# Kernel tuning notes

Measured on AMD Instinct MI355X. Metric: run time of the kernel, lower is better.

The kernel has to match this reference:

```python
import jax, jax.numpy as jnp
import numpy as np

MAX_STEPS = 50
B, H, A = 4096, 1024, 128


def setup_inputs() -> dict:
    key = jax.random.key(0)
    ks = jax.random.split(key, 7)
    s = 1.0 / np.sqrt(H)  # torch default LSTM/Linear init scale
    return {
        "encoder_output": jax.random.normal(ks[0], (1, B, H), dtype=jnp.float32),
        "w_ih": jax.random.normal(ks[1], (4 * H, H), dtype=jnp.float32) * s,
        "w_hh": jax.random.normal(ks[2], (4 * H, H), dtype=jnp.float32) * s,
        "b_ih": jax.random.normal(ks[3], (4 * H,), dtype=jnp.float32) * s,
        "b_hh": jax.random.normal(ks[4], (4 * H,), dtype=jnp.float32) * s,
        "w_pred": jax.random.normal(ks[5], (A, H), dtype=jnp.float32) * s,
        "b_pred": jax.random.normal(ks[6], (A,), dtype=jnp.float32) * s,
    }


def reference(encoder_output, w_ih, w_hh, b_ih, b_hh, w_pred, b_pred):
    # LSTM output (hidden state) of step t; seq_len is always 1.
    hidden = w_hh.shape[1]
    x0 = encoder_output[0]                        # (B, H)
    h0 = jnp.zeros_like(x0)
    c0 = jnp.zeros_like(x0)
    bias = b_ih + b_hh                            # (4H,)

    def step(carry, _):
        x, h, c = carry
        gates = x @ w_ih.T + h @ w_hh.T + bias    # (B, 4H)
        i, f, g, o = jnp.split(gates, 4, axis=-1)  # torch gate order i,f,g,o
        c_new = jax.nn.sigmoid(f) * c + jax.nn.sigmoid(i) * jnp.tanh(g)
        h_new = jax.nn.sigmoid(o) * jnp.tanh(c_new)
        p = h_new @ w_pred.T + b_pred             # (B, A)
        return (h_new, h_new, c_new), p

    _, predicted = jax.lax.scan(step, (x0, h0, c0), None, length=MAX_STEPS)
    return predicted  # (MAX_STEPS, B, A)
```

## Files before the change

kernel.cpp:

```cpp
#include <hip/hip_runtime.h>
#include <hip/hip_bf16.h>
#include <stdint.h>


#define B_SZ   4096
#define H_SZ   1024
#define A_SZ   128
#define NSTEP  50
#define NT     16
#define NTP    8

using bf16 = __hip_bfloat16;
typedef __attribute__((ext_vector_type(8))) short bf16x8;
typedef __attribute__((ext_vector_type(4))) float f32x4;

__device__ __forceinline__ void gload_lds16(const void* g, void* l) {
    __builtin_amdgcn_global_load_lds(
        (const __attribute__((address_space(1))) unsigned int*)g,
        (__attribute__((address_space(3))) unsigned int*)l, 16, 0, 0);
}

#define FENCE() asm volatile("" ::: "memory")
#define BAR()   do { FENCE(); __builtin_amdgcn_s_barrier(); FENCE(); } while (0)
#define VMC6()  asm volatile("s_waitcnt vmcnt(6)" ::: "memory")
#define VMC5()  asm volatile("s_waitcnt vmcnt(5)" ::: "memory")
#define VMC4()  asm volatile("s_waitcnt vmcnt(4)" ::: "memory")
#define VMC0()  asm volatile("s_waitcnt vmcnt(0)" ::: "memory")
#define LGKM0() asm volatile("s_waitcnt lgkmcnt(0)" ::: "memory")

__device__ __forceinline__ float sigf(float x) {
    return 1.f / (1.f + __expf(-x));
}
__device__ __forceinline__ float tanh_(float x) {
    float e = __expf(-2.f * fabsf(x));
    float t = (1.f - e) / (1.f + e);
    return copysignf(t, x);
}


__global__ void prep_all(const float4* __restrict__ wih,
                         const float4* __restrict__ whh,
                         bf16* __restrict__ Wc, bf16* __restrict__ Wi,
                         const float4* __restrict__ enc, bf16* __restrict__ encb,
                         const float4* __restrict__ wpred, bf16* __restrict__ wpb,
                         const float* __restrict__ bih, const float* __restrict__ bhh,
                         float* __restrict__ bias) {
    const int b = blockIdx.x;
    if (b < 4096) {
        int i = b * 256 + threadIdx.x;
        float4 a = wih[i], c = whh[i];
        bf16 tc[4] = {__float2bfloat16(a.x + c.x), __float2bfloat16(a.y + c.y),
                      __float2bfloat16(a.z + c.z), __float2bfloat16(a.w + c.w)};
        bf16 ti[4] = {__float2bfloat16(a.x), __float2bfloat16(a.y),
                      __float2bfloat16(a.z), __float2bfloat16(a.w)};
        *(uint64_t*)(Wc + 4 * (size_t)i) = *(const uint64_t*)tc;
        *(uint64_t*)(Wi + 4 * (size_t)i) = *(const uint64_t*)ti;
    } else if (b < 8192) {
        int i = (b - 4096) * 256 + threadIdx.x;
        float4 a = enc[i];
        bf16 t[4] = {__float2bfloat16(a.x), __float2bfloat16(a.y),
                     __float2bfloat16(a.z), __float2bfloat16(a.w)};
        *(uint64_t*)(encb + 4 * (size_t)i) = *(const uint64_t*)t;
    } else if (b < 8320) {
        int i = (b - 8192) * 256 + threadIdx.x;
        float4 a = wpred[i];
        bf16 t[4] = {__float2bfloat16(a.x), __float2bfloat16(a.y),
                     __float2bfloat16(a.z), __float2bfloat16(a.w)};
        *(uint64_t*)(wpb + 4 * (size_t)i) = *(const uint64_t*)t;
    } else {
        int i = (b - 8320) * 256 + threadIdx.x;
        bias[i] = bih[i] + bhh[i];
    }
}


__device__ __forceinline__ void pred_body(const bf16* __restrict__ h,
                                          const bf16* __restrict__ wp,
                                          const float* __restrict__ bp,
                                          float* __restrict__ pout,
                                          int pblk, int tid, bf16* sm) {
    bf16* const pH0 = sm;
    bf16* const pH1 = sm + 2048;
    bf16* const pP0 = sm + 4096;
    bf16* const pP1 = sm + 20480;

    const int w      = tid >> 6;
    const int lane   = tid & 63;
    const int lane15 = lane & 15;
    const int lhi    = lane >> 4;
    const int bm0    = pblk * 16;

    const int r   = tid >> 4;
    const int swb = ((tid & 15) * 16) ^ ((r & 7) << 4);
    const char* srcH = (const char*)h  + (size_t)(bm0 + (r & 15)) * 2048 + swb;
    const char* srcP = (const char*)wp + (size_t)r * 2048 + swb;

    int eoff[4];
#pragma unroll
    for (int kk = 0; kk < 4; ++kk)
        eoff[kk] = ((kk * 64 + lhi * 16) ^ ((lane15 & 7) << 4)) >> 1;

    f32x4 acc = {0.f, 0.f, 0.f, 0.f};

    auto STAGE = [&](int t) {
        bf16* dH = (t & 1) ? pH1 : pH0;
        bf16* dP = (t & 1) ? pP1 : pP0;
        if (w < 4)
            gload_lds16(srcH + (size_t)t * 256, dH + tid * 8);
#pragma unroll
        for (int q = 0; q < 4; ++q)
            gload_lds16(srcP + (size_t)q * 65536 + (size_t)t * 256, dP + q * 4096 + tid * 8);
    };

    STAGE(0);
#pragma unroll
    for (int t = 0; t < NTP; ++t) {
        if (t + 1 < NTP) {
            STAGE(t + 1);
            if (w < 4) { VMC5(); } else { VMC4(); }
        } else {
            VMC0();
        }
        BAR();
        const bf16* Hd = (t & 1) ? pH1 : pH0;
        const bf16* Pd = (t & 1) ? pP1 : pP0;
#pragma unroll
        for (int kk = 0; kk < 4; ++kk) {
            bf16x8 a = *(const bf16x8*)(Hd + lane15 * 128 + eoff[kk]);
            bf16x8 b = *(const bf16x8*)(Pd + (w * 16 + lane15) * 128 + eoff[kk]);
            acc = __builtin_amdgcn_mfma_f32_16x16x32_bf16(a, b, acc, 0, 0, 0);
        }
        BAR();
    }

    const int col = w * 16 + lane15;
    const float bpv = bp[col];
#pragma unroll
    for (int rr = 0; rr < 4; ++rr)
        pout[(size_t)(bm0 + lhi * 4 + rr) * A_SZ + col] = acc[rr] + bpv;
}


__global__ __launch_bounds__(512, 2)
void lstm_fused(const bf16* __restrict__ hin, const bf16* __restrict__ W,
                const float* __restrict__ bias, float* __restrict__ c,
                bf16* __restrict__ hout, int step0,
                const bf16* __restrict__ wp, const float* __restrict__ bp,
                float* __restrict__ pout) {
    __shared__ __align__(16) bf16 sm[65536];

    if (blockIdx.x >= 256) {
        if (pout) pred_body(hin, wp, bp, pout, blockIdx.x - 256, threadIdx.x, sm);
        return;
    }

    bf16* const lA0 = sm;
    bf16* const lA1 = sm + 16384;
    bf16* const lB0 = sm + 32768;
    bf16* const lB1 = sm + 49152;

    const int tid    = threadIdx.x;
    const int w      = tid >> 6;
    const int lane   = tid & 63;
    const int wr     = w >> 2;
    const int wc     = w & 3;
    const int lane15 = lane & 15;
    const int lhi    = lane >> 4;

    const int bid     = blockIdx.x;
    const int logical = (bid & 7) * 32 + (bid >> 3);
    const int bm0     = (logical >> 4) * 256;
    const int j0      = (logical & 15) * 64;

    const int scolb = ((tid & 7) * 16) ^ (((tid >> 3) & 7) << 4);
    const char* baseA = (const char*)hin + (size_t)(bm0 + (tid >> 3)) * 2048 + scolb;
    const char* baseB = (const char*)W   + (size_t)(j0  + (tid >> 3)) * 2048 + scolb;

    const int cs0 = ((     lhi * 16) ^ ((lane & 7) << 4)) >> 1;
    const int cs1 = ((64 + lhi * 16) ^ ((lane & 7) << 4)) >> 1;
    const int rA  = (wr * 128 + lane15) * 64;
    const int rB  = (wc * 16  + lane15) * 64;

    f32x4 acc[8][4];
    const f32x4 z = {0.f, 0.f, 0.f, 0.f};
#pragma unroll
    for (int m = 0; m < 8; ++m)
#pragma unroll
        for (int n = 0; n < 4; ++n) acc[m][n] = z;

    auto SGA = [&](int t, int h) {
        bf16* dst = ((t & 1) ? lA1 : lA0) + h * 8192 + w * 512;
        const char* g = baseA + (size_t)(h * 128) * 2048 + (size_t)t * 128;
        gload_lds16(g, dst);
        gload_lds16(g + (size_t)64 * 2048, dst + 4096);
    };
    auto SGB = [&](int t, int h) {
        bf16* dst = ((t & 1) ? lB1 : lB0) + h * 8192 + w * 512;
        const char* g = baseB + (size_t)(h * 2) * 2097152 + (size_t)t * 128;
        gload_lds16(g, dst);
        gload_lds16(g + 2097152, dst + 4096);
    };

    SGB(0, 0); SGB(0, 1); SGA(0, 0); SGA(0, 1);
    SGB(1, 0); SGB(1, 1); SGA(1, 0);

    VMC6();
    BAR();

    for (int t = 0; t < NT; ++t) {
        const bf16* Ad = (t & 1) ? lA1 : lA0;
        const bf16* Bd = (t & 1) ? lB1 : lB0;
        bf16x8 av[4][2], bv[4][2];

#pragma unroll
        for (int m = 0; m < 4; ++m) {
            av[m][0] = *(const bf16x8*)(Ad + rA + m * 1024 + cs0);
            av[m][1] = *(const bf16x8*)(Ad + rA + m * 1024 + cs1);
        }
#pragma unroll
        for (int n = 0; n < 2; ++n) {
            bv[n][0] = *(const bf16x8*)(Bd + rB + n * 4096 + cs0);
            bv[n][1] = *(const bf16x8*)(Bd + rB + n * 4096 + cs1);
        }
        if (t + 1 < NT) SGA(t + 1, 1);
        BAR(); LGKM0();
        __builtin_amdgcn_s_setprio(1);
#pragma unroll
        for (int n = 0; n < 2; ++n)
#pragma unroll
            for (int m = 0; m < 4; ++m) {
                acc[m][n] = __builtin_amdgcn_mfma_f32_16x16x32_bf16(av[m][0], bv[n][0], acc[m][n], 0, 0, 0);
                acc[m][n] = __builtin_amdgcn_mfma_f32_16x16x32_bf16(av[m][1], bv[n][1], acc[m][n], 0, 0, 0);
            }
        __builtin_amdgcn_s_setprio(0);
        BAR();

#pragma unroll
        for (int n = 2; n < 4; ++n) {
            bv[n][0] = *(const bf16x8*)(Bd + rB + n * 4096 + cs0);
            bv[n][1] = *(const bf16x8*)(Bd + rB + n * 4096 + cs1);
        }
        if (t + 2 < NT) SGB(t + 2, 0);
        BAR(); LGKM0();
        __builtin_amdgcn_s_setprio(1);
#pragma unroll
        for (int n = 2; n < 4; ++n)
#pragma unroll
            for (int m = 0; m < 4; ++m) {
                acc[m][n] = __builtin_amdgcn_mfma_f32_16x16x32_bf16(av[m][0], bv[n][0], acc[m][n], 0, 0, 0);
                acc[m][n] = __builtin_amdgcn_mfma_f32_16x16x32_bf16(av[m][1], bv[n][1], acc[m][n], 0, 0, 0);
            }
        __builtin_amdgcn_s_setprio(0);
        BAR();

#pragma unroll
        for (int m = 0; m < 4; ++m) {
            av[m][0] = *(const bf16x8*)(Ad + rA + (m + 4) * 1024 + cs0);
            av[m][1] = *(const bf16x8*)(Ad + rA + (m + 4) * 1024 + cs1);
        }
        if (t + 2 < NT) SGB(t + 2, 1);
        BAR(); LGKM0();
        __builtin_amdgcn_s_setprio(1);
#pragma unroll
        for (int n = 0; n < 2; ++n)
#pragma unroll
            for (int m = 0; m < 4; ++m) {
                acc[m + 4][n] = __builtin_amdgcn_mfma_f32_16x16x32_bf16(av[m][0], bv[n][0], acc[m + 4][n], 0, 0, 0);
                acc[m + 4][n] = __builtin_amdgcn_mfma_f32_16x16x32_bf16(av[m][1], bv[n][1], acc[m + 4][n], 0, 0, 0);
            }
        __builtin_amdgcn_s_setprio(0);
        BAR();

        if (t + 2 < NT) SGA(t + 2, 0);
        BAR(); LGKM0();
        __builtin_amdgcn_s_setprio(1);
#pragma unroll
        for (int n = 2; n < 4; ++n)
#pragma unroll
            for (int m = 0; m < 4; ++m) {
                acc[m + 4][n] = __builtin_amdgcn_mfma_f32_16x16x32_bf16(av[m][0], bv[n][0], acc[m + 4][n], 0, 0, 0);
                acc[m + 4][n] = __builtin_amdgcn_mfma_f32_16x16x32_bf16(av[m][1], bv[n][1], acc[m + 4][n], 0, 0, 0);
            }
        __builtin_amdgcn_s_setprio(0);
        if (t < NT - 1) {
            if (t == NT - 2) { VMC0(); } else { VMC6(); }
        }
        BAR();
    }

    const int jc = j0 + wc * 16 + lane15;
    const float bi  = bias[jc];
    const float bff = bias[H_SZ + jc];
    const float bg  = bias[2 * H_SZ + jc];
    const float bo  = bias[3 * H_SZ + jc];
#pragma unroll
    for (int m = 0; m < 8; ++m) {
#pragma unroll
        for (int r = 0; r < 4; ++r) {
            int row = bm0 + wr * 128 + m * 16 + lhi * 4 + r;
            size_t idx = (size_t)row * H_SZ + jc;
            float iv = acc[m][0][r] + bi;
            float fv = acc[m][1][r] + bff;
            float gv = acc[m][2][r] + bg;
            float ov = acc[m][3][r] + bo;
            float cp = step0 ? 0.f : c[idx];
            float cn = sigf(fv) * cp + sigf(iv) * tanh_(gv);
            float hn = sigf(ov) * tanh_(cn);
            c[idx] = cn;
            hout[idx] = __float2bfloat16(hn);
        }
    }
}


__global__ __launch_bounds__(512)
void pred_tail(const bf16* __restrict__ h, const bf16* __restrict__ wp,
               const float* __restrict__ bp, float* __restrict__ out) {
    __shared__ __align__(16) bf16 sm2[36864];
    pred_body(h, wp, bp, out, blockIdx.x, threadIdx.x, sm2);
}


extern "C" void kernel_launch(void* const* d_in, const int* in_sizes, int n_in,
                              void* d_out, int out_size, void* d_ws, size_t ws_size,
                              hipStream_t stream) {
    const float* enc   = (const float*)d_in[0];
    const float* wih   = (const float*)d_in[1];
    const float* whh   = (const float*)d_in[2];
    const float* bih   = (const float*)d_in[3];
    const float* bhh   = (const float*)d_in[4];
    const float* wpred = (const float*)d_in[5];
    const float* bpred = (const float*)d_in[6];
    float* out = (float*)d_out;

    char* ws = (char*)d_ws;
    const size_t WH = (size_t)4 * H_SZ * H_SZ;
    const size_t BH = (size_t)B_SZ * H_SZ;
    bf16*  Wc   = (bf16*)ws;                 ws += WH * 2;
    bf16*  Wi   = (bf16*)ws;                 ws += WH * 2;
    bf16*  h0   = (bf16*)ws;                 ws += BH * 2;
    bf16*  h1   = (bf16*)ws;                 ws += BH * 2;
    float* cbuf = (float*)ws;                ws += BH * 4;
    bf16*  wp   = (bf16*)ws;                 ws += (size_t)A_SZ * H_SZ * 2;
    float* bias = (float*)ws;                ws += 4 * H_SZ * 4;

    prep_all<<<8336, 256, 0, stream>>>((const float4*)wih, (const float4*)whh, Wc, Wi,
                                       (const float4*)enc, h0,
                                       (const float4*)wpred, wp,
                                       bih, bhh, bias);

    bf16* hbuf[2] = {h0, h1};
    for (int s = 0; s < NSTEP; ++s) {
        const bf16* hin = hbuf[s & 1];
        bf16* hout      = hbuf[(s + 1) & 1];
        float* pout = (s == 0) ? nullptr : out + (size_t)(s - 1) * (B_SZ * A_SZ);
        lstm_fused<<<512, 512, 0, stream>>>(
            hin, (s == 0) ? Wi : Wc, bias, cbuf, hout, s == 0 ? 1 : 0,
            wp, bpred, pout);
    }
    pred_tail<<<B_SZ / 16, 512, 0, stream>>>(
        hbuf[0], wp, bpred, out + (size_t)(NSTEP - 1) * (B_SZ * A_SZ));
}
```

Measured before the change: 2.327 ms.

## Peel last K-tile to overlap LSTM cell epilogue with MFMAs and prefetch c

Changes the block-to-tile mapping to a different interleave of batch and hidden indices, which alters L2/MALL locality across XCDs. The final K iteration is peeled out: the previous cell state c is prefetched into registers during the second-to-last iteration. The epilogue is split into two halves so the first half's gate math and stores run alongside the MFMAs for the second half. This is meant to hide c-load latency and epilogue time, at the cost of more registers (cpre[8][4]) and possible occupancy or spill pressure.

Result: slower. 2.438 ms (+4.8%).

```diff
diff --git a/kernel.cpp b/kernel.cpp
--- a/kernel.cpp
+++ b/kernel.cpp
@@ -167,10 +167,11 @@
     const int lane15 = lane & 15;
     const int lhi    = lane >> 4;
 
-    const int bid     = blockIdx.x;
-    const int logical = (bid & 7) * 32 + (bid >> 3);
-    const int bm0     = (logical >> 4) * 256;
-    const int j0      = (logical & 15) * 64;
+    const int bid    = blockIdx.x;
+    const int bm_idx = ((bid & 1) << 3) | ((bid >> 3) & 7);
+    const int j_idx  = (((bid >> 1) & 3) << 2) | ((bid >> 6) & 3);
+    const int bm0    = bm_idx * 256;
+    const int j0     = j_idx * 64;
 
     const int scolb = ((tid & 7) * 16) ^ (((tid >> 3) & 7) << 4);
     const char* baseA = (const char*)hin + (size_t)(bm0 + (tid >> 3)) * 2048 + scolb;
@@ -180,6 +181,8 @@
     const int cs1 = ((64 + lhi * 16) ^ ((lane & 7) << 4)) >> 1;
     const int rA  = (wr * 128 + lane15) * 64;
     const int rB  = (wc * 16  + lane15) * 64;
+
+    const int jc = j0 + wc * 16 + lane15;
 
     f32x4 acc[8][4];
     const f32x4 z = {0.f, 0.f, 0.f, 0.f};
@@ -207,7 +210,9 @@
     VMC6();
     BAR();
 
-    for (int t = 0; t < NT; ++t) {
+    float cpre[8][4];
+
+    for (int t = 0; t < NT - 1; ++t) {
         const bf16* Ad = (t & 1) ? lA1 : lA0;
         const bf16* Bd = (t & 1) ? lB1 : lB0;
         bf16x8 av[4][2], bv[4][2];
@@ -222,7 +227,7 @@
             bv[n][0] = *(const bf16x8*)(Bd + rB + n * 4096 + cs0);
             bv[n][1] = *(const bf16x8*)(Bd + rB + n * 4096 + cs1);
         }
-        if (t + 1 < NT) SGA(t + 1, 1);
+        SGA(t + 1, 1);
         BAR(); LGKM0();
         __builtin_amdgcn_s_setprio(1);
 #pragma unroll
@@ -282,33 +287,113 @@
                 acc[m + 4][n] = __builtin_amdgcn_mfma_f32_16x16x32_bf16(av[m][1], bv[n][1], acc[m + 4][n], 0, 0, 0);
             }
         __builtin_amdgcn_s_setprio(0);
-        if (t < NT - 1) {
-            if (t == NT - 2) { VMC0(); } else { VMC6(); }
-        }
-        BAR();
-    }
-
-    const int jc = j0 + wc * 16 + lane15;
+        if (t == NT - 2) {
+            VMC0();
+            if (!step0) {
+#pragma unroll
+                for (int m = 0; m < 8; ++m)
+#pragma unroll
+                    for (int r = 0; r < 4; ++r)
+                        cpre[m][r] = c[(size_t)(bm0 + wr * 128 + m * 16 + lhi * 4 + r) * H_SZ + jc];
+            } else {
+#pragma unroll
+                for (int m = 0; m < 8; ++m)
+#pragma unroll
+                    for (int r = 0; r < 4; ++r) cpre[m][r] = 0.f;
+            }
+        } else {
+            VMC6();
+        }
+        BAR();
+    }
+
     const float bi  = bias[jc];
     const float bff = bias[H_SZ + jc];
     const float bg  = bias[2 * H_SZ + jc];
     const float bo  = bias[3 * H_SZ + jc];
-#pragma unroll
-    for (int m = 0; m < 8; ++m) {
-#pragma unroll
-        for (int r = 0; r < 4; ++r) {
-            int row = bm0 + wr * 128 + m * 16 + lhi * 4 + r;
-            size_t idx = (size_t)row * H_SZ + jc;
-            float iv = acc[m][0][r] + bi;
-            float fv = acc[m][1][r] + bff;
-            float gv = acc[m][2][r] + bg;
-            float ov = acc[m][3][r] + bo;
-            float cp = step0 ? 0.f : c[idx];
-            float cn = sigf(fv) * cp + sigf(iv) * tanh_(gv);
-            float hn = sigf(ov) * tanh_(cn);
-            c[idx] = cn;
-            hout[idx] = __float2bfloat16(hn);
-        }
+
+    auto cell_half = [&](int mb) {
+#pragma unroll
+        for (int m = mb; m < mb + 4; ++m) {
+#pragma unroll
+            for (int r = 0; r < 4; ++r) {
+                int row = bm0 + wr * 128 + m * 16 + lhi * 4 + r;
+                size_t idx = (size_t)row * H_SZ + jc;
+                float iv = acc[m][0][r] + bi;
+                float fv = acc[m][1][r] + bff;
+                float gv = acc[m][2][r] + bg;
+                float ov = acc[m][3][r] + bo;
+                float cn = sigf(fv) * cpre[m][r] + sigf(iv) * tanh_(gv);
+                float hn = sigf(ov) * tanh_(cn);
+                c[idx] = cn;
+                hout[idx] = __float2bfloat16(hn);
+            }
+        }
+    };
+
+    {
+        const bf16* Ad = lA1;
+        const bf16* Bd = lB1;
+        bf16x8 av[4][2], bv[4][2];
+
+#pragma unroll
+        for (int m = 0; m < 4; ++m) {
+            av[m][0] = *(const bf16x8*)(Ad + rA + m * 1024 + cs0);
+            av[m][1] = *(const bf16x8*)(Ad + rA + m * 1024 + cs1);
+        }
+#pragma unroll
+        for (int n = 0; n < 2; ++n) {
+            bv[n][0] = *(const bf16x8*)(Bd + rB + n * 4096 + cs0);
+            bv[n][1] = *(const bf16x8*)(Bd + rB + n * 4096 + cs1);
+        }
+        LGKM0();
+        __builtin_amdgcn_s_setprio(1);
+#pragma unroll
+        for (int n = 0; n < 2; ++n)
+#pragma unroll
+            for (int m = 0; m < 4; ++m) {
+                acc[m][n] = __builtin_amdgcn_mfma_f32_16x16x32_bf16(av[m][0], bv[n][0], acc[m][n], 0, 0, 0);
+                acc[m][n] = __builtin_amdgcn_mfma_f32_16x16x32_bf16(av[m][1], bv[n][1], acc[m][n], 0, 0, 0);
+            }
+        __builtin_amdgcn_s_setprio(0);
+
+#pragma unroll
+        for (int n = 2; n < 4; ++n) {
+            bv[n][0] = *(const bf16x8*)(Bd + rB + n * 4096 + cs0);
+            bv[n][1] = *(const bf16x8*)(Bd + rB + n * 4096 + cs1);
+        }
+        LGKM0();
+        __builtin_amdgcn_s_setprio(1);
+#pragma unroll
+        for (int n = 2; n < 4; ++n)
+#pragma unroll
+            for (int m = 0; m < 4; ++m) {
+                acc[m][n] = __builtin_amdgcn_mfma_f32_16x16x32_bf16(av[m][0], bv[n][0], acc[m][n], 0, 0, 0);
+                acc[m][n] = __builtin_amdgcn_mfma_f32_16x16x32_bf16(av[m][1], bv[n][1], acc[m][n], 0, 0, 0);
+            }
+        __builtin_amdgcn_s_setprio(0);
+
+#pragma unroll
+        for (int m = 0; m < 4; ++m) {
+            av[m][0] = *(const bf16x8*)(Ad + rA + (m + 4) * 1024 + cs0);
+            av[m][1] = *(const bf16x8*)(Ad + rA + (m + 4) * 1024 + cs1);
+        }
+
+        VMC0();
+        cell_half(0);
+
+        LGKM0();
+        __builtin_amdgcn_s_setprio(1);
+#pragma unroll
+        for (int n = 0; n < 4; ++n)
+#pragma unroll
+            for (int m = 0; m < 4; ++m) {
+                acc[m + 4][n] = __builtin_amdgcn_mfma_f32_16x16x32_bf16(av[m][0], bv[n][0], acc[m + 4][n], 0, 0, 0);
+                acc[m + 4][n] = __builtin_amdgcn_mfma_f32_16x16x32_bf16(av[m][1], bv[n][1], acc[m + 4][n], 0, 0, 0);
+            }
+        __builtin_amdgcn_s_setprio(0);
+
+        cell_half(4);
     }
 }
 
```
